# Kernel optimization log

Hardware: AMD Instinct MI355X
Metric: run time of the kernel (lower is better)

## Reference

```python
import jax, jax.numpy as jnp
import numpy as np

NUM_HEADS = 16
THETA = 10000.0
B, S, D = 2, 2048, 1024
D_K = D // NUM_HEADS


def setup_inputs() -> dict:
    key = jax.random.key(0)
    ks = jax.random.split(key, 5)
    s = 0.02
    return {
        "x": jax.random.normal(ks[0], (B, S, D), dtype=jnp.float32),
        "W_q": jax.random.normal(ks[1], (D, D), dtype=jnp.float32) * s,
        "W_k": jax.random.normal(ks[2], (D, D), dtype=jnp.float32) * s,
        "W_v": jax.random.normal(ks[3], (D, D), dtype=jnp.float32) * s,
        "W_o": jax.random.normal(ks[4], (D, D), dtype=jnp.float32) * s,
        "token_positions": jnp.arange(S, dtype=jnp.int32),
    }


def _rope(x, token_positions):
    # x: [..., seq, d_k]; equivalent to the block-diagonal 2x2 rotation matmul
    d2 = x.shape[-1] // 2
    inv_freq = THETA ** (-(2.0 * jnp.arange(d2, dtype=x.dtype)) / x.shape[-1])  # [d2]
    ang = token_positions.astype(x.dtype)[:, None] * inv_freq[None, :]  # [seq, d2]
    cos, sin = jnp.cos(ang), jnp.sin(ang)
    xp = x.reshape(x.shape[:-1] + (d2, 2))
    xe, xo = xp[..., 0], xp[..., 1]
    oe = cos * xe - sin * xo
    oo = sin * xe + cos * xo
    return jnp.stack([oe, oo], axis=-1).reshape(x.shape)


def reference(x, W_q, W_k, W_v, W_o, token_positions):
    seq = x.shape[-2]
    # QKV projections (weights stored as [out, in])
    Q = jnp.einsum('bsd,ed->bse', x, W_q)
    K = jnp.einsum('bsd,ed->bse', x, W_k)
    V = jnp.einsum('bsd,ed->bse', x, W_v)
    def split_heads(t):
        return t.reshape(t.shape[:-1] + (NUM_HEADS, D_K)).swapaxes(-3, -2)  # [b,h,s,dk]
    Q, K, V = split_heads(Q), split_heads(K), split_heads(V)
    Q = _rope(Q, token_positions)
    K = _rope(K, token_positions)
    scale = 1.0 / np.sqrt(D_K)
    scores = jnp.einsum('bhqd,bhkd->bhqk', Q, K) * scale
    causal = jnp.tril(jnp.ones((seq, seq), dtype=bool))
    scores = jnp.where(causal, scores, -jnp.inf)
    probs = jax.nn.softmax(scores, axis=-1)
    out = jnp.einsum('bhqk,bhkd->bhqd', probs, V)
    out = out.swapaxes(-3, -2).reshape(x.shape[:-1] + (D,))
    return jnp.einsum('bse,de->bsd', out, W_o)
```

## Files before the change

### kernel.cpp

```cpp
#include <hip/hip_runtime.h>
#include <hip/hip_bf16.h>
#include <math.h>

#define H_    16
#define DK_   64
#define Dm    1024
#define Bb    2
#define Ss    2048
#define Mrows 4096
#define QSCALE 0.1803368801f

typedef short s16x8 __attribute__((ext_vector_type(8)));
typedef float f32x4 __attribute__((ext_vector_type(4)));
typedef unsigned short u16;
typedef unsigned int u32;

__device__ __forceinline__ u16 f2b(float f) {
  __hip_bfloat16 h = __float2bfloat16(f);
  return *reinterpret_cast<u16*>(&h);
}
__device__ __forceinline__ float b2f(u16 u) {
  __hip_bfloat16 h;
  *reinterpret_cast<u16*>(&h) = u;
  return __bfloat162float(h);
}
__device__ __forceinline__ u32 pkbf(float hi, float lo) {
  return __builtin_amdgcn_perm(__float_as_uint(hi), __float_as_uint(lo), 0x07060302u);
}

#define GLDS(g, l)                                                             \
  __builtin_amdgcn_global_load_lds(                                            \
      (const __attribute__((address_space(1))) unsigned int*)(g),              \
      (__attribute__((address_space(3))) unsigned int*)(l), 16, 0, 0)

__device__ __forceinline__ int SW64(int row, int col) {
  return row * 64 + ((((col >> 3) ^ (row & 7) ^ (row >> 3)) & 7) << 3) + (col & 7);
}

__global__ __launch_bounds__(256) void k_castall(
    const float* __restrict__ x,  const float* __restrict__ Wq,
    const float* __restrict__ Wk, const float* __restrict__ Wv,
    const float* __restrict__ Wo,
    u16* __restrict__ xb,  u16* __restrict__ wqb, u16* __restrict__ wkb,
    u16* __restrict__ wvb, u16* __restrict__ wob,
    const int* __restrict__ pos, float2* __restrict__ tab) {
  if (blockIdx.x >= 8192) {
    int t = (blockIdx.x - 8192) * 256 + threadIdx.x;
    int s = t >> 5, i = t & 31;
    float p = (float)pos[s];
    float ang = p * powf(10000.0f, -(float)i / 32.0f);
    tab[t] = make_float2(cosf(ang), sinf(ang));
    return;
  }
  int i = blockIdx.x * 256 + threadIdx.x;
  const float* s;
  u16* d;
  int off;
  if (i < 1048576) { s = x; d = xb; off = i; }
  else {
    int j = i - 1048576;
    int w = j >> 18;
    off = j & 262143;
    s = (w == 0) ? Wq : (w == 1) ? Wk : (w == 2) ? Wv : Wo;
    d = (w == 0) ? wqb : (w == 1) ? wkb : (w == 2) ? wvb : wob;
  }
  float4 v = reinterpret_cast<const float4*>(s)[off];
  ushort4 o;
  o.x = f2b(v.x); o.y = f2b(v.y); o.z = f2b(v.z); o.w = f2b(v.w);
  reinterpret_cast<ushort4*>(d)[off] = o;
}

__global__ __launch_bounds__(256) void k_ropeK(u16* __restrict__ K,
                                               const float2* __restrict__ tab) {
  int t = blockIdx.x * 256 + threadIdx.x;
  int row = t >> 7;
  int c0 = (t & 127) << 3;
  int i0 = (c0 & 63) >> 1;
  const float2* tb = &tab[(row & (Ss - 1)) * 32 + i0];
  float2 cs[4];
#pragma unroll
  for (int j = 0; j < 4; ++j) cs[j] = tb[j];
  size_t off = (size_t)row * Dm + c0;
  s16x8 k = *reinterpret_cast<const s16x8*>(&K[off]);
  s16x8 ko;
#pragma unroll
  for (int j = 0; j < 4; ++j) {
    float ke = b2f((u16)k[2 * j]), kd = b2f((u16)k[2 * j + 1]);
    ko[2 * j]     = (short)f2b(cs[j].x * ke - cs[j].y * kd);
    ko[2 * j + 1] = (short)f2b(cs[j].y * ke + cs[j].x * kd);
  }
  *reinterpret_cast<s16x8*>(&K[off]) = ko;
}

template <int BN, bool QKV>
__global__ __launch_bounds__(256) void k_gemm(
    const u16* __restrict__ A, const u16* __restrict__ B,
    u16* __restrict__ OQ, u16* __restrict__ OK2, u16* __restrict__ OVT,
    float* __restrict__ OF, int K) {
  constexpr int NFR = BN / 32;
  __shared__ __align__(16) u16 lsA[2][128 * 32];
  __shared__ __align__(16) u16 lsB[2][BN * 32];
  const int tid = threadIdx.x, lane = tid & 63, wave = tid >> 6;
  const int quad = lane >> 4, l16 = lane & 15;
  const int wrow = wave >> 1, wcol = wave & 1;
  const int n0 = blockIdx.x * BN, m0 = blockIdx.y * 128;
  f32x4 acc[4][NFR] = {};

  auto stage = [&](int k0, int bi) {
#pragma unroll
    for (int c = 0; c < 2; ++c) {
      int f = (wave * 2 + c) * 64 + lane;
      int row = f >> 2;
      int gs = (f & 3) ^ ((row >> 1) & 3);
      GLDS(A + (size_t)(m0 + row) * K + k0 + gs * 8, &lsA[bi][(wave * 2 + c) * 512]);
    }
#pragma unroll
    for (int c = 0; c < NFR / 2; ++c) {
      int f = (wave * (NFR / 2) + c) * 64 + lane;
      int row = f >> 2;
      int gs = (f & 3) ^ ((row >> 1) & 3);
      GLDS(B + (size_t)(n0 + row) * K + k0 + gs * 8, &lsB[bi][(wave * (NFR / 2) + c) * 512]);
    }
  };

  stage(0, 0);
  int bi = 0;
  for (int k0 = 0; k0 < K; k0 += 32) {
    __syncthreads();
    if (k0 + 32 < K) stage(k0 + 32, bi ^ 1);
    s16x8 af[4], bfr[NFR];
#pragma unroll
    for (int i = 0; i < 4; ++i) {
      int row = wrow * 64 + i * 16 + l16;
      af[i] = *reinterpret_cast<const s16x8*>(
          &lsA[bi][row * 32 + ((quad ^ ((row >> 1) & 3)) << 3)]);
    }
#pragma unroll
    for (int i = 0; i < NFR; ++i) {
      int row = wcol * (BN / 2) + i * 16 + l16;
      bfr[i] = *reinterpret_cast<const s16x8*>(
          &lsB[bi][row * 32 + ((quad ^ ((row >> 1) & 3)) << 3)]);
    }
#pragma unroll
    for (int mi = 0; mi < 4; ++mi)
#pragma unroll
      for (int ni = 0; ni < NFR; ++ni)
        acc[mi][ni] = __builtin_amdgcn_mfma_f32_16x16x32_bf16(af[mi], bfr[ni], acc[mi][ni], 0, 0, 0);
    bi ^= 1;
  }

  if (QKV) {
    const int which = n0 >> 10;
    const int nbase = (n0 & 1023) + wcol * (BN / 2);
    if (which == 2) {
#pragma unroll
      for (int mi = 0; mi < 4; ++mi)
#pragma unroll
        for (int ni = 0; ni < NFR; ++ni) {
          int row0 = m0 + wrow * 64 + mi * 16 + quad * 4;
          int col  = nbase + ni * 16 + l16;
          int bb = row0 >> 11, s0 = row0 & (Ss - 1);
          ushort4 pk;
          pk.x = f2b(acc[mi][ni][0]); pk.y = f2b(acc[mi][ni][1]);
          pk.z = f2b(acc[mi][ni][2]); pk.w = f2b(acc[mi][ni][3]);
          *reinterpret_cast<ushort4*>(&OVT[((size_t)bb * Dm + col) * Ss + s0]) = pk;
        }
    } else {
      u16* Op = which ? OK2 : OQ;
#pragma unroll
      for (int mi = 0; mi < 4; ++mi)
#pragma unroll
        for (int ni = 0; ni < NFR; ++ni)
#pragma unroll
          for (int r = 0; r < 4; ++r) {
            int row = m0 + wrow * 64 + mi * 16 + quad * 4 + r;
            int col = nbase + ni * 16 + l16;
            Op[(size_t)row * Dm + col] = f2b(acc[mi][ni][r]);
          }
    }
  } else {
#pragma unroll
    for (int mi = 0; mi < 4; ++mi)
#pragma unroll
      for (int ni = 0; ni < NFR; ++ni)
#pragma unroll
        for (int r = 0; r < 4; ++r) {
          int row = m0 + wrow * 64 + mi * 16 + quad * 4 + r;
          int col = n0 + wcol * (BN / 2) + ni * 16 + l16;
          OF[(size_t)row * Dm + col] = acc[mi][ni][r];
        }
  }
}

__device__ const signed char T_QT[24] = {15,15,14, 7,14,13,13,12, 6,12,11,11,
                                         10, 5,10, 9, 9, 8, 4, 8, 3, 2, 1, 0};
__device__ const signed char T_PS[24] = { 0, 8, 0, 0, 8, 0, 7, 0, 0, 7, 0, 6,
                                          0, 0, 6, 0, 5, 0, 0, 5, 0, 0, 0, 0};
__device__ const signed char T_PE[24] = { 8,16, 8, 8,15, 7,14, 7, 7,13, 6,12,
                                          6, 6,11, 5,10, 5, 5, 9, 4, 3, 2, 1};

__global__ __launch_bounds__(256) void k_flash(const u16* __restrict__ Q,
                                               const u16* __restrict__ K,
                                               const u16* __restrict__ VT,
                                               u16* __restrict__ O,
                                               const float2* __restrict__ tab,
                                               float* __restrict__ Op,
                                               float* __restrict__ Lp) {
  __shared__ __align__(16) u16 lsK[4][64 * 64];
  __shared__ __align__(16) u16 lsVT[4][64 * 64];
  __shared__ __align__(16) u16 lsP[4][32 * 64];
  const int tid = threadIdx.x, lane = tid & 63, wave = tid >> 6;
  const int quad = lane >> 4, l16 = lane & 15;
  const int bid = blockIdx.x;
  const int j = bid >> 5, bh = bid & 31;
  const int qt = T_QT[j];
  const int ps = T_PS[j], pe = T_PE[j];
  const int h = bh & (H_ - 1), b = bh >> 4;
  const int q0 = qt * 128;
  const int qbase = q0 + wave * 32;
  const int ktmax_w = (qbase + 31) >> 6;
  const int xorv = (l16 * 2) & 0xE;

  s16x8 qf[2][2];
#pragma unroll
  for (int s = 0; s < 2; ++s) {
    const int qpos = qbase + s * 16 + l16;
    const size_t qoff = (size_t)(b * Ss + qpos) * Dm + h * 64;
    s16x8 r0 = *reinterpret_cast<const s16x8*>(&Q[qoff + quad * 8]);
    s16x8 r1 = *reinterpret_cast<const s16x8*>(&Q[qoff + 32 + quad * 8]);
    const float2* tb = &tab[(qpos & (Ss - 1)) * 32];
#pragma unroll
    for (int kc = 0; kc < 2; ++kc) {
      s16x8 raw = kc ? r1 : r0;
#pragma unroll
      for (int p = 0; p < 4; ++p) {
        float2 cs = tb[kc * 16 + quad * 4 + p];
        float e = b2f((u16)raw[2 * p]), o = b2f((u16)raw[2 * p + 1]);
        qf[s][kc][2 * p]     = (short)f2b((cs.x * e - cs.y * o) * QSCALE);
        qf[s][kc][2 * p + 1] = (short)f2b((cs.y * e + cs.x * o) * QSCALE);
      }
    }
  }
  s16x8 ones;
#pragma unroll
  for (int j2 = 0; j2 < 8; ++j2) ones[j2] = (short)0x3F80;

  f32x4 ot[2][4] = {};
  f32x4 lAcc[2] = {};

  auto stagepair = [&](int pp) {
#pragma unroll
    for (int half = 0; half < 2; ++half) {
      const int kt = pp * 2 + half;
      const int slot = kt & 3;
      const size_t kbase  = (size_t)(b * Ss + kt * 64) * Dm + h * 64;
      const size_t vtbase = ((size_t)b * Dm + h * 64) * Ss + kt * 64;
#pragma unroll
      for (int c = 0; c < 2; ++c) {
        int sl = (wave * 2 + c) * 64 + lane;
        int row = sl >> 3;
        int gg = ((sl & 7) ^ (row & 7) ^ (row >> 3)) & 7;
        GLDS(K  + kbase  + (size_t)row * Dm + gg * 8, &lsK[slot][(wave * 2 + c) * 512]);
        GLDS(VT + vtbase + (size_t)row * Ss + gg * 8, &lsVT[slot][(wave * 2 + c) * 512]);
      }
    }
  };

  stagepair(ps);
  for (int pp = ps; pp < pe; ++pp) {
    __syncthreads();
    if (pp + 1 < pe) stagepair(pp + 1);
    const int kt0 = 2 * pp;

    f32x4 st[2][2][4] = {};
#pragma unroll
    for (int half = 0; half < 2; ++half) {
      const int kt = kt0 + half;
      if (kt > ktmax_w) break;
      const int slot = kt & 3;
#pragma unroll
      for (int kc = 0; kc < 2; ++kc)
#pragma unroll
        for (int ni = 0; ni < 4; ++ni) {
          s16x8 kf = *reinterpret_cast<const s16x8*>(
              &lsK[slot][SW64(ni * 16 + l16, kc * 32 + quad * 8)]);
          st[half][0][ni] = __builtin_amdgcn_mfma_f32_16x16x32_bf16(kf, qf[0][kc], st[half][0][ni], 0, 0, 0);
          st[half][1][ni] = __builtin_amdgcn_mfma_f32_16x16x32_bf16(kf, qf[1][kc], st[half][1][ni], 0, 0, 0);
        }
    }
#pragma unroll
    for (int half = 0; half < 2; ++half) {
      const int kt = kt0 + half;
      if (kt > ktmax_w) break;
      const int slot = kt & 3;
      if (kt == ktmax_w) {
#pragma unroll
        for (int s = 0; s < 2; ++s) {
          int gq = qbase + s * 16 + l16;
#pragma unroll
          for (int ni = 0; ni < 4; ++ni)
#pragma unroll
            for (int r = 0; r < 4; ++r)
              if (kt * 64 + ni * 16 + quad * 4 + r > gq) st[half][s][ni][r] = -INFINITY;
        }
      }
#pragma unroll
      for (int s = 0; s < 2; ++s)
#pragma unroll
        for (int ni = 0; ni < 4; ++ni) {
          float e0 = __builtin_amdgcn_exp2f(st[half][s][ni][0]);
          float e1 = __builtin_amdgcn_exp2f(st[half][s][ni][1]);
          float e2 = __builtin_amdgcn_exp2f(st[half][s][ni][2]);
          float e3 = __builtin_amdgcn_exp2f(st[half][s][ni][3]);
          uint2 pk;
          pk.x = pkbf(e1, e0);
          pk.y = pkbf(e3, e2);
          *reinterpret_cast<uint2*>(
              &lsP[wave][(s * 16 + l16) * 64 + (((ni * 4 + quad) ^ xorv) << 2)]) = pk;
        }
#pragma unroll
      for (int kc = 0; kc < 2; ++kc) {
        s16x8 pf0 = *reinterpret_cast<const s16x8*>(
            &lsP[wave][l16 * 64 + (((kc * 8 + quad * 2) ^ xorv) << 2)]);
        s16x8 pf1 = *reinterpret_cast<const s16x8*>(
            &lsP[wave][(16 + l16) * 64 + (((kc * 8 + quad * 2) ^ xorv) << 2)]);
        lAcc[0] = __builtin_amdgcn_mfma_f32_16x16x32_bf16(ones, pf0, lAcc[0], 0, 0, 0);
        lAcc[1] = __builtin_amdgcn_mfma_f32_16x16x32_bf16(ones, pf1, lAcc[1], 0, 0, 0);
#pragma unroll
        for (int ni = 0; ni < 4; ++ni) {
          s16x8 vf = *reinterpret_cast<const s16x8*>(
              &lsVT[slot][SW64(ni * 16 + l16, kc * 32 + quad * 8)]);
          ot[0][ni] = __builtin_amdgcn_mfma_f32_16x16x32_bf16(vf, pf0, ot[0][ni], 0, 0, 0);
          ot[1][ni] = __builtin_amdgcn_mfma_f32_16x16x32_bf16(vf, pf1, ot[1][ni], 0, 0, 0);
        }
      }
    }
  }

  if (ps == 0 && pe == qt + 1) {
#pragma unroll
    for (int s = 0; s < 2; ++s) {
      float inv = 1.0f / lAcc[s][0];
      const size_t obase = (size_t)(b * Ss + qbase + s * 16 + l16) * Dm + h * 64;
#pragma unroll
      for (int ni = 0; ni < 4; ++ni) {
        ushort4 pk;
        pk.x = f2b(ot[s][ni][0] * inv); pk.y = f2b(ot[s][ni][1] * inv);
        pk.z = f2b(ot[s][ni][2] * inv); pk.w = f2b(ot[s][ni][3] * inv);
        *reinterpret_cast<ushort4*>(&O[obase + ni * 16 + quad * 4]) = pk;
      }
    }
  } else {
    const int part = ps ? 1 : 0;
    const int slot = ((bh << 3) + (qt - 8)) * 2 + part;
    float* Ob = Op + (size_t)slot * 8192;
    float* Lb = Lp + slot * 128;
#pragma unroll
    for (int s = 0; s < 2; ++s) {
      int qi = wave * 32 + s * 16 + l16;
      if (quad == 0) Lb[qi] = lAcc[s][0];
#pragma unroll
      for (int ni = 0; ni < 4; ++ni)
        *reinterpret_cast<f32x4*>(&Ob[(size_t)qi * 64 + ni * 16 + quad * 4]) = ot[s][ni];
    }
  }
}

__global__ __launch_bounds__(256) void k_combine(const float* __restrict__ Op,
                                                 const float* __restrict__ Lp,
                                                 u16* __restrict__ O) {
  int t = blockIdx.x * 256 + threadIdx.x;
  int dk4 = t & 15, qi = (t >> 4) & 127, tile = t >> 11;
  int bh = tile >> 3, qt = 8 + (tile & 7);
  int slot = tile * 2;
  const float* O0 = Op + (size_t)slot * 8192;
  const float* O1 = Op + (size_t)(slot + 1) * 8192;
  float inv = 1.0f / (Lp[slot * 128 + qi] + Lp[(slot + 1) * 128 + qi]);
  f32x4 a = *reinterpret_cast<const f32x4*>(&O0[(size_t)qi * 64 + dk4 * 4]);
  f32x4 c = *reinterpret_cast<const f32x4*>(&O1[(size_t)qi * 64 + dk4 * 4]);
  int b = bh >> 4, h = bh & (H_ - 1);
  size_t obase = (size_t)(b * Ss + qt * 128 + qi) * Dm + h * 64;
  ushort4 pk;
  pk.x = f2b((a[0] + c[0]) * inv); pk.y = f2b((a[1] + c[1]) * inv);
  pk.z = f2b((a[2] + c[2]) * inv); pk.w = f2b((a[3] + c[3]) * inv);
  *reinterpret_cast<ushort4*>(&O[obase + dk4 * 4]) = pk;
}

extern "C" void kernel_launch(void* const* d_in, const int* in_sizes, int n_in,
                              void* d_out, int out_size, void* d_ws, size_t ws_size,
                              hipStream_t stream) {
  const float* x  = (const float*)d_in[0];
  const float* Wq = (const float*)d_in[1];
  const float* Wk = (const float*)d_in[2];
  const float* Wv = (const float*)d_in[3];
  const float* Wo = (const float*)d_in[4];
  const int* pos  = (const int*)d_in[5];
  float* out = (float*)d_out;

  char* w = (char*)d_ws;
  u16* xb  = (u16*)w; w += (size_t)Mrows * Dm * 2;
  u16* wqb = (u16*)w; w += (size_t)Dm * Dm * 2;
  u16* wkb = (u16*)w; w += (size_t)Dm * Dm * 2;
  u16* wvb = (u16*)w; w += (size_t)Dm * Dm * 2;
  u16* wob = (u16*)w; w += (size_t)Dm * Dm * 2;
  u16* Qb  = (u16*)w; w += (size_t)Mrows * Dm * 2;
  u16* Kb  = (u16*)w; w += (size_t)Mrows * Dm * 2;
  u16* VTb = (u16*)w; w += (size_t)Mrows * Dm * 2;
  u16* Ab  = (u16*)w; w += (size_t)Mrows * Dm * 2;
  float2* tabf = (float2*)w; w += (size_t)Ss * 32 * sizeof(float2);
  float* op = (float*)d_out;
  float* lp = (float*)xb;

  k_castall<<<8448, 256, 0, stream>>>(x, Wq, Wk, Wv, Wo, xb, wqb, wkb, wvb, wob,
                                      pos, tabf);
  k_gemm<128, true><<<dim3(24, 32), 256, 0, stream>>>(xb, wqb, Qb, Kb, VTb, nullptr, Dm);
  k_ropeK<<<Mrows * Dm / 8 / 256, 256, 0, stream>>>(Kb, tabf);
  k_flash<<<dim3(768), 256, 0, stream>>>(Qb, Kb, VTb, Ab, tabf, op, lp);
  k_combine<<<2048, 256, 0, stream>>>(op, lp, Ab);
  k_gemm<64, false><<<dim3(16, 32), 256, 0, stream>>>(Ab, wob, nullptr, nullptr, nullptr, out, Dm);
}
```

Measured before the change: 192.6 us.

## Stage one K/V tile per iteration with double buffering and reorder split schedule

Replaces the pair-of-tiles staging with a four-slot LDS ring by single 64-key tile staging into a two-slot ring, so each iteration does one QK, softmax and PV step. This halves K/V shared memory, which may allow more resident blocks per CU. The block-to-work schedule tables are also reordered so heavy and split query tiles are interleaved differently across the launch. The cost is one barrier per tile instead of per pair and less prefetch depth, so load latency may be exposed more.

```diff
diff --git a/kernel.cpp b/kernel.cpp
--- a/kernel.cpp
+++ b/kernel.cpp
@@ -192,12 +192,15 @@
   }
 }
 
-__device__ const signed char T_QT[24] = {15,15,14, 7,14,13,13,12, 6,12,11,11,
-                                         10, 5,10, 9, 9, 8, 4, 8, 3, 2, 1, 0};
-__device__ const signed char T_PS[24] = { 0, 8, 0, 0, 8, 0, 7, 0, 0, 7, 0, 6,
-                                          0, 0, 6, 0, 5, 0, 0, 5, 0, 0, 0, 0};
-__device__ const signed char T_PE[24] = { 8,16, 8, 8,15, 7,14, 7, 7,13, 6,12,
-                                          6, 6,11, 5,10, 5, 5, 9, 4, 3, 2, 1};
+__device__ const signed char T_QT[24] = {15,14, 7,13,13,12, 6,10,
+                                         15,14,12,11,11,10, 9, 5,
+                                          0, 1, 2, 8, 3, 9, 4, 8};
+__device__ const signed char T_PS[24] = { 0, 0, 0, 0, 7, 0, 0, 0,
+                                          8, 8, 7, 0, 6, 6, 5, 0,
+                                          0, 0, 0, 5, 0, 0, 0, 0};
+__device__ const signed char T_PE[24] = { 8, 8, 8, 7,14, 7, 7, 6,
+                                         16,15,13, 6,12,11,10, 6,
+                                          1, 2, 3, 9, 4, 5, 5, 5};
 
 __global__ __launch_bounds__(256) void k_flash(const u16* __restrict__ Q,
                                                const u16* __restrict__ K,
@@ -206,8 +209,8 @@
                                                const float2* __restrict__ tab,
                                                float* __restrict__ Op,
                                                float* __restrict__ Lp) {
-  __shared__ __align__(16) u16 lsK[4][64 * 64];
-  __shared__ __align__(16) u16 lsVT[4][64 * 64];
+  __shared__ __align__(16) u16 lsK[2][64 * 64];
+  __shared__ __align__(16) u16 lsVT[2][64 * 64];
   __shared__ __align__(16) u16 lsP[4][32 * 64];
   const int tid = threadIdx.x, lane = tid & 63, wave = tid >> 6;
   const int quad = lane >> 4, l16 = lane & 15;
@@ -248,91 +251,78 @@
   f32x4 ot[2][4] = {};
   f32x4 lAcc[2] = {};
 
-  auto stagepair = [&](int pp) {
-#pragma unroll
-    for (int half = 0; half < 2; ++half) {
-      const int kt = pp * 2 + half;
-      const int slot = kt & 3;
-      const size_t kbase  = (size_t)(b * Ss + kt * 64) * Dm + h * 64;
-      const size_t vtbase = ((size_t)b * Dm + h * 64) * Ss + kt * 64;
-#pragma unroll
-      for (int c = 0; c < 2; ++c) {
-        int sl = (wave * 2 + c) * 64 + lane;
-        int row = sl >> 3;
-        int gg = ((sl & 7) ^ (row & 7) ^ (row >> 3)) & 7;
-        GLDS(K  + kbase  + (size_t)row * Dm + gg * 8, &lsK[slot][(wave * 2 + c) * 512]);
-        GLDS(VT + vtbase + (size_t)row * Ss + gg * 8, &lsVT[slot][(wave * 2 + c) * 512]);
-      }
+  auto stage1 = [&](int kt) {
+    const int slot = kt & 1;
+    const size_t kbase  = (size_t)(b * Ss + kt * 64) * Dm + h * 64;
+    const size_t vtbase = ((size_t)b * Dm + h * 64) * Ss + kt * 64;
+#pragma unroll
+    for (int c = 0; c < 2; ++c) {
+      int sl = (wave * 2 + c) * 64 + lane;
+      int row = sl >> 3;
+      int gg = ((sl & 7) ^ (row & 7) ^ (row >> 3)) & 7;
+      GLDS(K  + kbase  + (size_t)row * Dm + gg * 8, &lsK[slot][(wave * 2 + c) * 512]);
+      GLDS(VT + vtbase + (size_t)row * Ss + gg * 8, &lsVT[slot][(wave * 2 + c) * 512]);
     }
   };
 
-  stagepair(ps);
-  for (int pp = ps; pp < pe; ++pp) {
+  const int kt_s = ps * 2, kt_e = pe * 2;
+  stage1(kt_s);
+  for (int kt = kt_s; kt < kt_e; ++kt) {
     __syncthreads();
-    if (pp + 1 < pe) stagepair(pp + 1);
-    const int kt0 = 2 * pp;
-
-    f32x4 st[2][2][4] = {};
-#pragma unroll
-    for (int half = 0; half < 2; ++half) {
-      const int kt = kt0 + half;
-      if (kt > ktmax_w) break;
-      const int slot = kt & 3;
-#pragma unroll
-      for (int kc = 0; kc < 2; ++kc)
-#pragma unroll
-        for (int ni = 0; ni < 4; ++ni) {
-          s16x8 kf = *reinterpret_cast<const s16x8*>(
-              &lsK[slot][SW64(ni * 16 + l16, kc * 32 + quad * 8)]);
-          st[half][0][ni] = __builtin_amdgcn_mfma_f32_16x16x32_bf16(kf, qf[0][kc], st[half][0][ni], 0, 0, 0);
-          st[half][1][ni] = __builtin_amdgcn_mfma_f32_16x16x32_bf16(kf, qf[1][kc], st[half][1][ni], 0, 0, 0);
-        }
-    }
-#pragma unroll
-    for (int half = 0; half < 2; ++half) {
-      const int kt = kt0 + half;
-      if (kt > ktmax_w) break;
-      const int slot = kt & 3;
-      if (kt == ktmax_w) {
-#pragma unroll
-        for (int s = 0; s < 2; ++s) {
-          int gq = qbase + s * 16 + l16;
-#pragma unroll
-          for (int ni = 0; ni < 4; ++ni)
-#pragma unroll
-            for (int r = 0; r < 4; ++r)
-              if (kt * 64 + ni * 16 + quad * 4 + r > gq) st[half][s][ni][r] = -INFINITY;
-        }
-      }
-#pragma unroll
-      for (int s = 0; s < 2; ++s)
-#pragma unroll
-        for (int ni = 0; ni < 4; ++ni) {
-          float e0 = __builtin_amdgcn_exp2f(st[half][s][ni][0]);
-          float e1 = __builtin_amdgcn_exp2f(st[half][s][ni][1]);
-          float e2 = __builtin_amdgcn_exp2f(st[half][s][ni][2]);
-          float e3 = __builtin_amdgcn_exp2f(st[half][s][ni][3]);
-          uint2 pk;
-          pk.x = pkbf(e1, e0);
-          pk.y = pkbf(e3, e2);
-          *reinterpret_cast<uint2*>(
-              &lsP[wave][(s * 16 + l16) * 64 + (((ni * 4 + quad) ^ xorv) << 2)]) = pk;
-        }
-#pragma unroll
-      for (int kc = 0; kc < 2; ++kc) {
-        s16x8 pf0 = *reinterpret_cast<const s16x8*>(
-            &lsP[wave][l16 * 64 + (((kc * 8 + quad * 2) ^ xorv) << 2)]);
-        s16x8 pf1 = *reinterpret_cast<const s16x8*>(
-            &lsP[wave][(16 + l16) * 64 + (((kc * 8 + quad * 2) ^ xorv) << 2)]);
-        lAcc[0] = __builtin_amdgcn_mfma_f32_16x16x32_bf16(ones, pf0, lAcc[0], 0, 0, 0);
-        lAcc[1] = __builtin_amdgcn_mfma_f32_16x16x32_bf16(ones, pf1, lAcc[1], 0, 0, 0);
-#pragma unroll
-        for (int ni = 0; ni < 4; ++ni) {
-          s16x8 vf = *reinterpret_cast<const s16x8*>(
-              &lsVT[slot][SW64(ni * 16 + l16, kc * 32 + quad * 8)]);
-          ot[0][ni] = __builtin_amdgcn_mfma_f32_16x16x32_bf16(vf, pf0, ot[0][ni], 0, 0, 0);
-          ot[1][ni] = __builtin_amdgcn_mfma_f32_16x16x32_bf16(vf, pf1, ot[1][ni], 0, 0, 0);
-        }
+    if (kt + 1 < kt_e) stage1(kt + 1);
+    if (kt > ktmax_w) continue;
+    const int slot = kt & 1;
+
+    f32x4 st[2][4] = {};
+#pragma unroll
+    for (int kc = 0; kc < 2; ++kc)
+#pragma unroll
+      for (int ni = 0; ni < 4; ++ni) {
+        s16x8 kf = *reinterpret_cast<const s16x8*>(
+            &lsK[slot][SW64(ni * 16 + l16, kc * 32 + quad * 8)]);
+        st[0][ni] = __builtin_amdgcn_mfma_f32_16x16x32_bf16(kf, qf[0][kc], st[0][ni], 0, 0, 0);
+        st[1][ni] = __builtin_amdgcn_mfma_f32_16x16x32_bf16(kf, qf[1][kc], st[1][ni], 0, 0, 0);
+      }
+
+    if (kt == ktmax_w) {
+#pragma unroll
+      for (int s = 0; s < 2; ++s) {
+        int gq = qbase + s * 16 + l16;
+#pragma unroll
+        for (int ni = 0; ni < 4; ++ni)
+#pragma unroll
+          for (int r = 0; r < 4; ++r)
+            if (kt * 64 + ni * 16 + quad * 4 + r > gq) st[s][ni][r] = -INFINITY;
+      }
+    }
+#pragma unroll
+    for (int s = 0; s < 2; ++s)
+#pragma unroll
+      for (int ni = 0; ni < 4; ++ni) {
+        float e0 = __builtin_amdgcn_exp2f(st[s][ni][0]);
+        float e1 = __builtin_amdgcn_exp2f(st[s][ni][1]);
+        float e2 = __builtin_amdgcn_exp2f(st[s][ni][2]);
+        float e3 = __builtin_amdgcn_exp2f(st[s][ni][3]);
+        uint2 pk;
+        pk.x = pkbf(e1, e0);
+        pk.y = pkbf(e3, e2);
+        *reinterpret_cast<uint2*>(
+            &lsP[wave][(s * 16 + l16) * 64 + (((ni * 4 + quad) ^ xorv) << 2)]) = pk;
+      }
+#pragma unroll
+    for (int kc = 0; kc < 2; ++kc) {
+      s16x8 pf0 = *reinterpret_cast<const s16x8*>(
+          &lsP[wave][l16 * 64 + (((kc * 8 + quad * 2) ^ xorv) << 2)]);
+      s16x8 pf1 = *reinterpret_cast<const s16x8*>(
+          &lsP[wave][(16 + l16) * 64 + (((kc * 8 + quad * 2) ^ xorv) << 2)]);
+      lAcc[0] = __builtin_amdgcn_mfma_f32_16x16x32_bf16(ones, pf0, lAcc[0], 0, 0, 0);
+      lAcc[1] = __builtin_amdgcn_mfma_f32_16x16x32_bf16(ones, pf1, lAcc[1], 0, 0, 0);
+#pragma unroll
+      for (int ni = 0; ni < 4; ++ni) {
+        s16x8 vf = *reinterpret_cast<const s16x8*>(
+            &lsVT[slot][SW64(ni * 16 + l16, kc * 32 + quad * 8)]);
+        ot[0][ni] = __builtin_amdgcn_mfma_f32_16x16x32_bf16(vf, pf0, ot[0][ni], 0, 0, 0);
+        ot[1][ni] = __builtin_amdgcn_mfma_f32_16x16x32_bf16(vf, pf1, ot[1][ni], 0, 0, 0);
       }
     }
   }
```

Result: no change. 194.5 us (+1.0%).
